# Kernel tuning notes

Hardware: AMD Instinct MI355X
Metric: run time of the kernel (lower is better)

## Reference

```python
import jax, jax.numpy as jnp
import numpy as np


def setup_inputs() -> dict:
    key = jax.random.key(0)
    k1, k2 = jax.random.split(key)
    N, C = 16384, 4096
    x = jax.random.normal(k1, (N, C), dtype=jnp.float32)
    y = jax.random.randint(k2, (N, C), 0, 2, dtype=jnp.int64)
    return {"x": x, "y": y}


def reference(x, y):
    # Original loss: for each row i,
    #   loss_i = 1/(ni*(C-ni)) * sum_{j: y=1, k: y=0} exp(-(x_k - x_j))
    # which factorizes exactly into separable masked row sums:
    #   loss_i = (sum_{y=1} exp(x)) * (sum_{y=0} exp(-x)) / (ni*(C-ni))
    C = x.shape[1]
    m = (y == 1)
    pos = jnp.sum(jnp.where(m, jnp.exp(x), 0.0), axis=1)   # sum exp(x) over y==1
    neg = jnp.sum(jnp.where(m, 0.0, jnp.exp(-x)), axis=1)  # sum exp(-x) over y==0
    ni = jnp.sum(m, axis=1).astype(x.dtype)
    loss = jnp.mean(pos * neg / (ni * (C - ni)))
    return loss
```

## Files before the change

kernel.cpp:

```cpp
#include <hip/hip_runtime.h>


typedef float v4f __attribute__((ext_vector_type(4)));
typedef int   v4i __attribute__((ext_vector_type(4)));

#define C_DIM 4096
#define BLOCK 256
#define NBLK  2048
#define WPB   (BLOCK / 64)
#define RPW   2

__global__ __launch_bounds__(BLOCK) void pdl_rows(const float* __restrict__ x,
                                                  const int* __restrict__ y,
                                                  float* __restrict__ partial) {
    const int lane  = threadIdx.x & 63;
    const int wave  = threadIdx.x >> 6;
    const int gwave = blockIdx.x * WPB + wave;
    const int rbase = gwave * RPW;

    float pos = 0.0f, neg = 0.0f;
    int cnt = 0;
    float wacc = 0.0f;

    v4f xa[4], xb[4];
    v4i ya[4], yb[4];

    auto prefetch = [&](v4f (&xv)[4], v4i (&yv)[4], int c) {
        const size_t rowoff = (size_t)(rbase + (c >> 2)) * C_DIM;
        const v4f* __restrict__ x4 = (const v4f*)(x + rowoff);
        const v4i* __restrict__ y4 = (const v4i*)(y + rowoff);
#pragma unroll
        for (int u = 0; u < 4; ++u) {
            const int i = lane + ((c & 3) * 4 + u) * 64;
            xv[u] = __builtin_nontemporal_load(x4 + i);
            yv[u] = __builtin_nontemporal_load(y4 + i);
        }
    };
    auto compute = [&](const v4f (&xv)[4], const v4i (&yv)[4]) {
#pragma unroll
        for (int u = 0; u < 4; ++u) {
#pragma unroll
            for (int e = 0; e < 4; ++e) {
                const int   yy = yv[u][e];
                const float xx = xv[u][e];
                const float ex = __expf(yy ? xx : -xx);
                pos += yy ? ex : 0.0f;
                neg += yy ? 0.0f : ex;
                cnt += yy;
            }
        }
    };
    auto finish_row = [&]() {
#pragma unroll
        for (int off = 32; off >= 1; off >>= 1) {
            pos += __shfl_down(pos, off, 64);
            neg += __shfl_down(neg, off, 64);
            cnt += __shfl_down(cnt, off, 64);
        }
        if (lane == 0) {
            const float denom = (float)cnt * (float)(C_DIM - cnt);
            wacc += (pos * neg) / denom;
        }
        pos = 0.0f; neg = 0.0f; cnt = 0;
    };

    prefetch(xa, ya, 0);
    prefetch(xb, yb, 1);
    compute(xa, ya);  prefetch(xa, ya, 2);
    compute(xb, yb);  prefetch(xb, yb, 3);
    compute(xa, ya);  prefetch(xa, ya, 4);
    compute(xb, yb);  prefetch(xb, yb, 5);
    finish_row();
    compute(xa, ya);  prefetch(xa, ya, 6);
    compute(xb, yb);  prefetch(xb, yb, 7);
    compute(xa, ya);
    compute(xb, yb);
    finish_row();

    __shared__ float sacc[WPB];
    if (lane == 0) sacc[wave] = wacc;
    __syncthreads();
    if (threadIdx.x == 0) {
        float b = 0.0f;
#pragma unroll
        for (int w = 0; w < WPB; ++w) b += sacc[w];
        partial[blockIdx.x] = b;
    }
}

__global__ __launch_bounds__(BLOCK) void pdl_reduce(const float* __restrict__ partial,
                                                    float* __restrict__ out,
                                                    int n_partial, float inv_n) {
    const float4* p4 = (const float4*)partial;
    float s = 0.0f;
    for (int i = threadIdx.x; i < n_partial / 4; i += BLOCK) {
        const float4 v = p4[i];
        s += (v.x + v.y) + (v.z + v.w);
    }
#pragma unroll
    for (int off = 32; off >= 1; off >>= 1) s += __shfl_down(s, off, 64);
    __shared__ float sw[BLOCK / 64];
    const int lane = threadIdx.x & 63;
    const int wave = threadIdx.x >> 6;
    if (lane == 0) sw[wave] = s;
    __syncthreads();
    if (threadIdx.x == 0) {
        float t = 0.0f;
#pragma unroll
        for (int w = 0; w < BLOCK / 64; ++w) t += sw[w];
        out[0] = t * inv_n;
    }
}

extern "C" void kernel_launch(void* const* d_in, const int* in_sizes, int n_in,
                              void* d_out, int out_size, void* d_ws, size_t ws_size,
                              hipStream_t stream) {
    const float* x = (const float*)d_in[0];
    const int*   y = (const int*)d_in[1];
    float* out = (float*)d_out;
    float* partial = (float*)d_ws;

    const int n_rows = in_sizes[0] / C_DIM;

    pdl_rows<<<NBLK, BLOCK, 0, stream>>>(x, y, partial);
    pdl_reduce<<<1, BLOCK, 0, stream>>>(partial, out, NBLK, 1.0f / (float)n_rows);
}
```

Measured before the change: 466.9 us.

## Split into mask-packing kernel and x-reduction kernel using bit-packed labels

Adds a first kernel that reads the int32 labels and packs them into 64-bit ballot masks stored in workspace, and a second kernel that streams x and reads the compact mask instead of the full label array. This splits one fused streaming pass into two passes. Total DRAM traffic is not reduced, since y is still read in full and the mask adds an extra write and read. It also adds a kernel launch plus per-element shuffles to pull out the mask bits, so the likely effect is extra work with no bandwidth saving. The original fused kernel is kept as a fallback when the workspace is too small.

```diff
diff --git a/kernel.cpp b/kernel.cpp
--- a/kernel.cpp
+++ b/kernel.cpp
@@ -3,12 +3,110 @@
 
 typedef float v4f __attribute__((ext_vector_type(4)));
 typedef int   v4i __attribute__((ext_vector_type(4)));
+typedef unsigned long long u64;
 
 #define C_DIM 4096
 #define BLOCK 256
 #define NBLK  2048
 #define WPB   (BLOCK / 64)
 #define RPW   2
+#define GROUPS 16
+#define WPR    64
+
+__global__ __launch_bounds__(BLOCK) void pdl_mask(const int* __restrict__ y,
+                                                  u64* __restrict__ mask) {
+    const int lane  = threadIdx.x & 63;
+    const int wave  = threadIdx.x >> 6;
+    const int gwave = blockIdx.x * WPB + wave;
+    const int rbase = gwave * RPW;
+
+#pragma unroll
+    for (int r = 0; r < RPW; ++r) {
+        const int row = rbase + r;
+        const v4i* __restrict__ y4 = (const v4i*)(y + (size_t)row * C_DIM);
+        u64* __restrict__ mrow = mask + (size_t)row * WPR;
+
+        v4i b0 = __builtin_nontemporal_load(y4 + lane);
+        v4i b1 = __builtin_nontemporal_load(y4 + lane + 64);
+#pragma unroll
+        for (int k = 0; k < GROUPS; ++k) {
+            const v4i v = (k & 1) ? b1 : b0;
+            if (k + 2 < GROUPS) {
+                if (k & 1) b1 = __builtin_nontemporal_load(y4 + lane + (k + 2) * 64);
+                else       b0 = __builtin_nontemporal_load(y4 + lane + (k + 2) * 64);
+            }
+            const u64 w0 = __ballot(v[0] != 0);
+            const u64 w1 = __ballot(v[1] != 0);
+            const u64 w2 = __ballot(v[2] != 0);
+            const u64 w3 = __ballot(v[3] != 0);
+            const u64 w = (lane == 0) ? w0 : (lane == 1) ? w1 : (lane == 2) ? w2 : w3;
+            if (lane < 4) mrow[k * 4 + lane] = w;
+        }
+    }
+}
+
+__global__ __launch_bounds__(BLOCK) void pdl_x(const float* __restrict__ x,
+                                               const u64* __restrict__ mask,
+                                               float* __restrict__ partial) {
+    const int lane  = threadIdx.x & 63;
+    const int wave  = threadIdx.x >> 6;
+    const int gwave = blockIdx.x * WPB + wave;
+    const int rbase = gwave * RPW;
+
+    float wacc = 0.0f;
+
+#pragma unroll
+    for (int r = 0; r < RPW; ++r) {
+        const int row = rbase + r;
+        const v4f* __restrict__ x4 = (const v4f*)(x + (size_t)row * C_DIM);
+
+        const u64 myw = mask[(size_t)row * WPR + lane];
+
+        float pos = 0.0f, neg = 0.0f;
+
+        v4f b0 = __builtin_nontemporal_load(x4 + lane);
+        v4f b1 = __builtin_nontemporal_load(x4 + lane + 64);
+#pragma unroll
+        for (int k = 0; k < GROUPS; ++k) {
+            const v4f v = (k & 1) ? b1 : b0;
+            if (k + 2 < GROUPS) {
+                if (k & 1) b1 = __builtin_nontemporal_load(x4 + lane + (k + 2) * 64);
+                else       b0 = __builtin_nontemporal_load(x4 + lane + (k + 2) * 64);
+            }
+#pragma unroll
+            for (int e = 0; e < 4; ++e) {
+                const u64 w = __shfl(myw, k * 4 + e, 64);
+                const int bit = (int)((w >> lane) & 1ull);
+                const float xx = v[e];
+                const float ex = __expf(bit ? xx : -xx);
+                pos += bit ? ex : 0.0f;
+                neg += bit ? 0.0f : ex;
+            }
+        }
+
+        int cnt = __popcll(myw);
+#pragma unroll
+        for (int off = 32; off >= 1; off >>= 1) {
+            pos += __shfl_down(pos, off, 64);
+            neg += __shfl_down(neg, off, 64);
+            cnt += __shfl_down(cnt, off, 64);
+        }
+        if (lane == 0) {
+            const float denom = (float)cnt * (float)(C_DIM - cnt);
+            wacc += (pos * neg) / denom;
+        }
+    }
+
+    __shared__ float sacc[WPB];
+    if (lane == 0) sacc[wave] = wacc;
+    __syncthreads();
+    if (threadIdx.x == 0) {
+        float b = 0.0f;
+#pragma unroll
+        for (int w = 0; w < WPB; ++w) b += sacc[w];
+        partial[blockIdx.x] = b;
+    }
+}
 
 __global__ __launch_bounds__(BLOCK) void pdl_rows(const float* __restrict__ x,
                                                   const int* __restrict__ y,
@@ -119,9 +217,16 @@
     const int*   y = (const int*)d_in[1];
     float* out = (float*)d_out;
     float* partial = (float*)d_ws;
+    u64*   mask    = (u64*)((char*)d_ws + 8192);
 
     const int n_rows = in_sizes[0] / C_DIM;
-
-    pdl_rows<<<NBLK, BLOCK, 0, stream>>>(x, y, partial);
+    const size_t need = 8192 + (size_t)n_rows * WPR * sizeof(u64);
+
+    if (ws_size >= need) {
+        pdl_mask<<<NBLK, BLOCK, 0, stream>>>(y, mask);
+        pdl_x<<<NBLK, BLOCK, 0, stream>>>(x, mask, partial);
+    } else {
+        pdl_rows<<<NBLK, BLOCK, 0, stream>>>(x, y, partial);
+    }
     pdl_reduce<<<1, BLOCK, 0, stream>>>(partial, out, NBLK, 1.0f / (float)n_rows);
 }
```

Result: slower. 483.1 us (+3.5%).
